# Optimization experiments

Measured on AMD Instinct MI355X. Metric: run time of the kernel, lower is better.

Reference implementation:

```python
import jax, jax.numpy as jnp
import numpy as np

S, B, SD, OD = 10, 256, 16, 8
H = 10 * (SD * SD + OD * OD)        # 3200, gru hidden
OUT1 = 4 * SD * OD                  # 512
IN = 2 * (SD + OD)                  # 48
TEMP = 0.1                          # concrete-dropout temperature


def setup_inputs() -> dict:
    key = jax.random.key(0)
    ks = jax.random.split(key, 24)
    sc = lambda k, sh, s=0.05: jax.random.normal(k, sh, jnp.float32) * s
    return {
        "y_t": sc(ks[0], (B, OD), 1.0),
        "x_filtered_prev": sc(ks[1], (B, SD), 1.0),
        "x_filtered_prev_prev": sc(ks[2], (B, SD), 1.0),
        "y_prev": sc(ks[3], (B, OD), 1.0),
        "delta_x_prev": sc(ks[4], (B, SD), 1.0),
        "h_prev_ensemble": sc(ks[5], (S, B, H)),
        "F_mat": sc(ks[6], (SD, SD), 0.2),
        "H_mat": sc(ks[7], (OD, SD), 0.2),
        "fc_in_w": sc(ks[8], (H, IN)),
        "fc_in_b": jnp.zeros((H,), jnp.float32),
        "W_ih": sc(ks[9], (3 * H, H), 0.01),
        "W_hh": sc(ks[10], (3 * H, H), 0.01),
        "b_ih": jnp.zeros((3 * H,), jnp.float32),
        "b_hh": jnp.zeros((3 * H,), jnp.float32),
        "fc1_w": sc(ks[11], (OUT1, H)),
        "fc1_b": jnp.zeros((OUT1,), jnp.float32),
        "fc2_w": sc(ks[12], (SD * OD, OUT1)),
        "fc2_b": jnp.zeros((SD * OD,), jnp.float32),
        "p_logit1": jnp.array([0.5], jnp.float32),   # sigmoid -> p in (0.5, 0.8) range
        "p_logit2": jnp.array([1.0], jnp.float32),
        "u1": jax.random.uniform(ks[13], (S, B, H), jnp.float32, 1e-4, 1.0 - 1e-4),
        "u2": jax.random.uniform(ks[14], (S, B, OUT1), jnp.float32, 1e-4, 1.0 - 1e-4),
    }


def _concrete_dropout(x, u, p):
    # relaxed Bernoulli drop mask, scaled to keep expectation
    z = jax.nn.sigmoid((jnp.log(p) - jnp.log1p(-p) + jnp.log(u) - jnp.log1p(-u)) / TEMP)
    return x * (1.0 - z) / (1.0 - p)


def reference(y_t, x_filtered_prev, x_filtered_prev_prev, y_prev, delta_x_prev,
              h_prev_ensemble, F_mat, H_mat, fc_in_w, fc_in_b,
              W_ih, W_hh, b_ih, b_hh, fc1_w, fc1_b, fc2_w, fc2_b,
              p_logit1, p_logit2, u1, u2):
    # system model prediction (nonlinear f, linear h), vectorized over batch
    x_predicted = jnp.tanh(x_filtered_prev @ F_mat.T)          # (B, SD)
    y_predicted = x_predicted @ H_mat.T                        # (B, OD)

    residual = y_t - y_predicted
    diff_state = x_filtered_prev - x_filtered_prev_prev
    inp = jnp.concatenate([delta_x_prev, residual, diff_state, y_prev], axis=-1)  # (B, IN)
    a = jax.nn.relu(inp @ fc_in_w.T + fc_in_b)                 # (B, H) shared across ensemble

    p1 = jax.nn.sigmoid(p_logit1[0])
    p2 = jax.nn.sigmoid(p_logit2[0])

    def gru_cell(x, h):
        gx = x @ W_ih.T + b_ih
        gh = h @ W_hh.T + b_hh
        gx_r, gx_z, gx_n = jnp.split(gx, 3, axis=-1)
        gh_r, gh_z, gh_n = jnp.split(gh, 3, axis=-1)
        r = jax.nn.sigmoid(gx_r + gh_r)
        z = jax.nn.sigmoid(gx_z + gh_z)
        n = jnp.tanh(gx_n + r * gh_n)
        return (1.0 - z) * n + z * h

    def sample_fn(h_i, u1_i, u2_i):
        x = _concrete_dropout(a, u1_i, p1)                     # (B, H)
        h_new = gru_cell(x, h_i)                               # (B, H)
        o = jax.nn.relu(h_new @ fc1_w.T + fc1_b)               # (B, OUT1)
        o = _concrete_dropout(o, u2_i, p2)
        K = (o @ fc2_w.T + fc2_b).reshape(B, SD, OD)           # Kalman gain
        correction = jnp.einsum('bso,bo->bs', K, residual)
        return x_predicted + correction, h_new

    xf_ens, h_new_ens = jax.vmap(sample_fn)(h_prev_ensemble, u1, u2)  # (S,B,SD),(S,B,H)

    x_filtered_final = xf_ens.mean(axis=0)                     # (B, SD)
    diff = xf_ens - x_filtered_final                           # (S, B, SD)
    P_filtered_final = jnp.einsum('sbi,sbj->bij', diff, diff) / S

    # concrete-dropout regularizer (identical per ensemble member)
    ent = lambda p: p * jnp.log(p) + (1.0 - p) * jnp.log1p(-p)
    reg = (jnp.sum(fc_in_w ** 2) / (1.0 - p1) + H * ent(p1)
           + jnp.sum(fc1_w ** 2) / (1.0 - p2) + OUT1 * ent(p2))
    raw_regularization = jnp.full((S,), reg)

    return x_filtered_final, P_filtered_final, raw_regularization
```

## Files before the change

### kernel.cpp

```cpp
#include <hip/hip_runtime.h>
#include <hip/hip_bf16.h>
#include <math.h>

#define S_ENS 10
#define B_DIM 256
#define SD 16
#define OD 8
#define H_DIM 3200
#define OUT1 512
#define IN_DIM 48
#define M_ROWS (S_ENS * B_DIM)
#define TEMP_INV 10.0f

typedef unsigned short u16;
typedef __attribute__((ext_vector_type(8))) short short8;
typedef __attribute__((ext_vector_type(4))) short short4v;
typedef __attribute__((ext_vector_type(4))) float floatx4;

__device__ __forceinline__ float sigmoidf_(float x) { return 1.0f / (1.0f + __expf(-x)); }
__device__ __forceinline__ float fast_tanh(float x) {
    x = fminf(fmaxf(x, -15.f), 15.f);
    float e = __expf(2.f * x);
    return (e - 1.f) / (e + 1.f);
}

__device__ __forceinline__ u16 f2bf(float f) {
    union { float f; unsigned u; } v; v.f = f;
    unsigned u = v.u + 0x7fffu + ((v.u >> 16) & 1u);
    return (u16)(u >> 16);
}
__device__ __forceinline__ float bf2f(u16 h) {
    union { unsigned u; float f; } v; v.u = ((unsigned)h) << 16;
    return v.f;
}

__device__ __forceinline__ void gld_lds16(const u16* g, u16* l) {
    __builtin_amdgcn_global_load_lds((const __attribute__((address_space(1))) void*)g,
                                     (__attribute__((address_space(3))) void*)l, 16, 0, 0);
}

__device__ __forceinline__ void bar_() {
    __builtin_amdgcn_sched_barrier(0);
    asm volatile("" ::: "memory");
    __builtin_amdgcn_s_barrier();
    asm volatile("" ::: "memory");
    __builtin_amdgcn_sched_barrier(0);
}
#define VMCNT8() asm volatile("s_waitcnt vmcnt(8)" ::: "memory")

__device__ __forceinline__ void kloop128(
    const u16* __restrict__ A0, const u16* __restrict__ A1,
    const u16* __restrict__ B0, const u16* __restrict__ B1,
    int nts, int nt, int m_base, int n_base,
    u16* sA, u16* sB, floatx4 (&acc)[4][4])
{
    const int tid = threadIdx.x;
    const int wave = tid >> 6, lane = tid & 63;
    const int r = tid >> 2, c = tid & 3;
    const int swe = (c ^ ((r >> 1) & 3)) << 3;
    const int frow = lane & 15, fch = lane >> 4;
    const int wrow0 = (wave >> 1) * 64, wcol0 = (wave & 1) * 64;
    int aoff[4], boff[4];
    #pragma unroll
    for (int mi = 0; mi < 4; ++mi) {
        int row = wrow0 + mi * 16 + frow;
        aoff[mi] = row * 32 + ((fch ^ ((row >> 1) & 3)) << 3);
    }
    #pragma unroll
    for (int ni = 0; ni < 4; ++ni) {
        int row = wcol0 + ni * 16 + frow;
        boff[ni] = row * 32 + ((fch ^ ((row >> 1) & 3)) << 3);
    }

    auto stA = [&](int tau) {
        int tc = tau < nt ? tau : nt - 1;
        const u16* p = (tc < nts) ? A0 : A1;
        int k = ((tc < nts) ? tc : tc - nts) << 6;
        const u16* src = p + (size_t)(m_base + r) * H_DIM + swe + k;
        u16* dst = sA + (tc & 1) * 8192 + wave * 512;
        gld_lds16(src, dst);
        gld_lds16(src + (size_t)64 * H_DIM, dst + 2048);
        gld_lds16(src + 32, dst + 4096);
        gld_lds16(src + 32 + (size_t)64 * H_DIM, dst + 6144);
    };
    auto stB = [&](int tau) {
        int tc = tau < nt ? tau : nt - 1;
        const u16* p = (tc < nts) ? B0 : B1;
        int k = ((tc < nts) ? tc : tc - nts) << 6;
        const u16* src = p + (size_t)(n_base + r) * H_DIM + swe + k;
        u16* dst = sB + (tc & 1) * 8192 + wave * 512;
        gld_lds16(src, dst);
        gld_lds16(src + (size_t)64 * H_DIM, dst + 2048);
        gld_lds16(src + 32, dst + 4096);
        gld_lds16(src + 32 + (size_t)64 * H_DIM, dst + 6144);
    };

    stA(0); stB(0); stA(1); stB(1);
    VMCNT8();
    bar_();

    for (int t = 0; t < nt; ++t) {
        const int bo = (t & 1) * 8192;
        short8 af[4][2], bfr[4][2];
        #pragma unroll
        for (int mi = 0; mi < 4; ++mi) {
            af[mi][0] = *(const short8*)(sA + bo + aoff[mi]);
            af[mi][1] = *(const short8*)(sA + bo + 4096 + aoff[mi]);
        }
        #pragma unroll
        for (int ni = 0; ni < 2; ++ni) {
            bfr[ni][0] = *(const short8*)(sB + bo + boff[ni]);
            bfr[ni][1] = *(const short8*)(sB + bo + 4096 + boff[ni]);
        }
        #pragma unroll
        for (int ni = 2; ni < 4; ++ni) {
            bfr[ni][0] = *(const short8*)(sB + bo + boff[ni]);
            bfr[ni][1] = *(const short8*)(sB + bo + 4096 + boff[ni]);
        }
        bar_();
        __builtin_amdgcn_s_setprio(1);
        #pragma unroll
        for (int mi = 0; mi < 4; ++mi)
            #pragma unroll
            for (int ni = 0; ni < 2; ++ni) {
                acc[mi][ni] = __builtin_amdgcn_mfma_f32_16x16x32_bf16(af[mi][0], bfr[ni][0], acc[mi][ni], 0, 0, 0);
                acc[mi][ni] = __builtin_amdgcn_mfma_f32_16x16x32_bf16(af[mi][1], bfr[ni][1], acc[mi][ni], 0, 0, 0);
            }
        __builtin_amdgcn_s_setprio(0);
        bar_();
        stA(t + 2);
        stB(t + 2);
        __builtin_amdgcn_s_setprio(1);
        #pragma unroll
        for (int mi = 0; mi < 4; ++mi)
            #pragma unroll
            for (int ni = 2; ni < 4; ++ni) {
                acc[mi][ni] = __builtin_amdgcn_mfma_f32_16x16x32_bf16(af[mi][0], bfr[ni][0], acc[mi][ni], 0, 0, 0);
                acc[mi][ni] = __builtin_amdgcn_mfma_f32_16x16x32_bf16(af[mi][1], bfr[ni][1], acc[mi][ni], 0, 0, 0);
            }
        __builtin_amdgcn_s_setprio(0);
        VMCNT8();
        bar_();
    }
}

__global__ __launch_bounds__(256) void gru_gemm_a(
    const u16* __restrict__ Xbf, const u16* __restrict__ Hpbf,
    const u16* __restrict__ Wih, const u16* __restrict__ Whh,
    const float* __restrict__ b_ih, const float* __restrict__ b_hh,
    u16* __restrict__ Rb, u16* __restrict__ Zb, u16* __restrict__ Gb) {
    __shared__ u16 sA[16384], sB[16384];
    floatx4 acc[4][4];
    #pragma unroll
    for (int i = 0; i < 4; ++i)
        #pragma unroll
        for (int j = 0; j < 4; ++j) acc[i][j] = (floatx4){0.f, 0.f, 0.f, 0.f};
    const int g = blockIdx.z;
    const int bmi = blockIdx.x, nbi = blockIdx.y;
    const int m_base = bmi * 128, nb = nbi * 128;
    const size_t gstride = (size_t)H_DIM * H_DIM;
    if (g < 2) {
        kloop128(Xbf, Hpbf, Wih + g * gstride, Whh + g * gstride, 50, 100, m_base, nb, sA, sB, acc);
    } else {
        kloop128(Hpbf, Hpbf, Whh + 2 * gstride, Whh + 2 * gstride, 50, 50, m_base, nb, sA, sB, acc);
    }
    u16* outp = (g == 0) ? Rb : (g == 1) ? Zb : Gb;
    const int lane = threadIdx.x & 63, wave = threadIdx.x >> 6;
    const int wcol0 = (wave & 1) * 64, cc = lane & 15;
    const size_t tbase = (size_t)(nbi * 20 + bmi) * 16384 + wave * 4096 + lane * 4;
    #pragma unroll
    for (int ni = 0; ni < 4; ++ni) {
        int col = nb + wcol0 + ni * 16 + cc;
        float bsum;
        if (g == 0)      bsum = b_ih[col] + b_hh[col];
        else if (g == 1) bsum = b_ih[H_DIM + col] + b_hh[H_DIM + col];
        else             bsum = b_hh[2 * H_DIM + col];
        #pragma unroll
        for (int mi = 0; mi < 4; ++mi) {
            short4v o;
            #pragma unroll
            for (int j = 0; j < 4; ++j) {
                float v = acc[mi][ni][j] + bsum;
                if (g < 2) v = sigmoidf_(v);
                o[j] = (short)f2bf(v);
            }
            *(short4v*)(outp + tbase + (mi * 4 + ni) * 256) = o;
        }
    }
}

__global__ __launch_bounds__(256) void gru_gemm_b(
    const u16* __restrict__ Xbf, const u16* __restrict__ Wih,
    const u16* __restrict__ Rb, const u16* __restrict__ Zb, const u16* __restrict__ Gb,
    const float* __restrict__ b_ih,
    const float* __restrict__ hprev, u16* __restrict__ Hn) {
    __shared__ u16 sA[16384], sB[16384];
    floatx4 acc[4][4];
    #pragma unroll
    for (int i = 0; i < 4; ++i)
        #pragma unroll
        for (int j = 0; j < 4; ++j) acc[i][j] = (floatx4){0.f, 0.f, 0.f, 0.f};
    const int bmi = blockIdx.x, nbi = blockIdx.y;
    const int m_base = bmi * 128, nb = nbi * 128;
    const u16* Wn = Wih + (size_t)2 * H_DIM * H_DIM;
    kloop128(Xbf, Xbf, Wn, Wn, 50, 50, m_base, nb, sA, sB, acc);
    const int lane = threadIdx.x & 63, wave = threadIdx.x >> 6;
    const int wrow0 = (wave >> 1) * 64, wcol0 = (wave & 1) * 64;
    const int quad = lane >> 4, cc = lane & 15;
    const size_t tbase = (size_t)(nbi * 20 + bmi) * 16384 + wave * 4096 + lane * 4;
    #pragma unroll
    for (int ni = 0; ni < 4; ++ni) {
        int col = nb + wcol0 + ni * 16 + cc;
        float bin_ = b_ih[2 * H_DIM + col];
        #pragma unroll
        for (int mi = 0; mi < 4; ++mi) {
            size_t pidx = tbase + (mi * 4 + ni) * 256;
            short4v rv = *(const short4v*)(Rb + pidx);
            short4v zv = *(const short4v*)(Zb + pidx);
            short4v gv = *(const short4v*)(Gb + pidx);
            int rw = m_base + wrow0 + mi * 16 + quad * 4;
            #pragma unroll
            for (int j = 0; j < 4; ++j) {
                float r = bf2f((u16)rv[j]);
                float z = bf2f((u16)zv[j]);
                float gh = bf2f((u16)gv[j]);
                float n = fast_tanh(acc[mi][ni][j] + bin_ + r * gh);
                size_t idx = (size_t)(rw + j) * H_DIM + col;
                float h = hprev[idx];
                Hn[idx] = f2bf((1.f - z) * n + z * h);
            }
        }
    }
}

__global__ __launch_bounds__(256) void fc1_k(
    const u16* __restrict__ Hn, const u16* __restrict__ Wb,
    const float* __restrict__ bias, const float* __restrict__ u2,
    const float* __restrict__ pl2, float* __restrict__ O) {
    __shared__ u16 sA[4096], sB[2048];
    floatx4 acc[4][2];
    #pragma unroll
    for (int i = 0; i < 4; ++i) { acc[i][0] = (floatx4){0.f,0.f,0.f,0.f}; acc[i][1] = (floatx4){0.f,0.f,0.f,0.f}; }
    const int tid = threadIdx.x;
    const int wave = tid >> 6, lane = tid & 63;
    const int m_base = blockIdx.y * 128, nb = blockIdx.x * 64;
    const int r = tid >> 2, c = tid & 3;
    const int swe = (c ^ ((r >> 1) & 3)) << 3;
    const u16* Ag = Hn + (size_t)(m_base + r) * H_DIM + swe;
    const u16* Bg = Wb + (size_t)(nb + r) * H_DIM + swe;
    u16* sA0 = sA + wave * 512;
    u16* sB0 = sB + wave * 512;
    const int frow = lane & 15, fch = lane >> 4;
    const int wrow0 = (wave >> 1) * 64, wcol0 = (wave & 1) * 32;
    int aoff[4], boff[2];
    #pragma unroll
    for (int mi = 0; mi < 4; ++mi) {
        int row = wrow0 + mi * 16 + frow;
        aoff[mi] = row * 32 + ((fch ^ ((row >> 1) & 3)) << 3);
    }
    #pragma unroll
    for (int ni = 0; ni < 2; ++ni) {
        int row = wcol0 + ni * 16 + frow;
        boff[ni] = row * 32 + ((fch ^ ((row >> 1) & 3)) << 3);
    }
    for (int kk = 0; kk < 100; ++kk) {
        __syncthreads();
        gld_lds16(Ag + kk * 32, sA0);
        gld_lds16(Ag + kk * 32 + (size_t)64 * H_DIM, sA0 + 2048);
        gld_lds16(Bg + kk * 32, sB0);
        __syncthreads();
        short8 af[4], bfr[2];
        #pragma unroll
        for (int mi = 0; mi < 4; ++mi) af[mi] = *(const short8*)(sA + aoff[mi]);
        #pragma unroll
        for (int ni = 0; ni < 2; ++ni) bfr[ni] = *(const short8*)(sB + boff[ni]);
        #pragma unroll
        for (int mi = 0; mi < 4; ++mi)
            #pragma unroll
            for (int ni = 0; ni < 2; ++ni)
                acc[mi][ni] = __builtin_amdgcn_mfma_f32_16x16x32_bf16(af[mi], bfr[ni], acc[mi][ni], 0, 0, 0);
    }
    float p = sigmoidf_(pl2[0]);
    float lp = __logf(p) - log1pf(-p);
    float inv = 1.0f / (1.0f - p);
    const int quad = lane >> 4, cc = lane & 15;
    #pragma unroll
    for (int ni = 0; ni < 2; ++ni) {
        int col = nb + wcol0 + ni * 16 + cc;
        float bcol = bias[col];
        #pragma unroll
        for (int mi = 0; mi < 4; ++mi) {
            int rw = m_base + wrow0 + mi * 16 + quad * 4;
            #pragma unroll
            for (int j = 0; j < 4; ++j) {
                size_t idx = (size_t)(rw + j) * OUT1 + col;
                float v = fmaxf(acc[mi][ni][j] + bcol, 0.f);
                float u = u2[idx];
                float z = sigmoidf_((lp + __logf(u) - log1pf(-u)) * TEMP_INV);
                O[idx] = v * (1.0f - z) * inv;
            }
        }
    }
}

__global__ void cvt_bf16_k(const float* __restrict__ src, u16* __restrict__ dst, int n8) {
    int i = blockIdx.x * 256 + threadIdx.x;
    if (i >= n8) return;
    float4 v0 = *((const float4*)src + 2 * (size_t)i);
    float4 v1 = *((const float4*)src + 2 * (size_t)i + 1);
    short8 o;
    o[0] = (short)f2bf(v0.x); o[1] = (short)f2bf(v0.y);
    o[2] = (short)f2bf(v0.z); o[3] = (short)f2bf(v0.w);
    o[4] = (short)f2bf(v1.x); o[5] = (short)f2bf(v1.y);
    o[6] = (short)f2bf(v1.z); o[7] = (short)f2bf(v1.w);
    *(short8*)(dst + 8 * (size_t)i) = o;
}

__global__ void prep_k(const float* __restrict__ y_t, const float* __restrict__ xfp,
                       const float* __restrict__ xfpp, const float* __restrict__ yprev,
                       const float* __restrict__ dxp, const float* __restrict__ Fm,
                       const float* __restrict__ Hm,
                       float* __restrict__ xpred, float* __restrict__ resid,
                       float* __restrict__ inp) {
    int b = threadIdx.x;
    float xrow[SD], xp[SD];
    for (int k = 0; k < SD; ++k) xrow[k] = xfp[b * SD + k];
    for (int s = 0; s < SD; ++s) {
        float acc = 0.f;
        for (int k = 0; k < SD; ++k) acc += xrow[k] * Fm[s * SD + k];
        xp[s] = tanhf(acc);
        xpred[b * SD + s] = xp[s];
    }
    float res[OD];
    for (int o = 0; o < OD; ++o) {
        float acc = 0.f;
        for (int s = 0; s < SD; ++s) acc += xp[s] * Hm[o * SD + s];
        res[o] = y_t[b * OD + o] - acc;
        resid[b * OD + o] = res[o];
    }
    float* ir = inp + b * IN_DIM;
    for (int k = 0; k < SD; ++k) ir[k] = dxp[b * SD + k];
    for (int o = 0; o < OD; ++o) ir[SD + o] = res[o];
    for (int k = 0; k < SD; ++k) ir[SD + OD + k] = xrow[k] - xfpp[b * SD + k];
    for (int o = 0; o < OD; ++o) ir[SD + OD + SD + o] = yprev[b * OD + o];
}

__global__ void fc_in_k(const float* __restrict__ inp, const float* __restrict__ w,
                        const float* __restrict__ bias, float* __restrict__ a) {
    int b = blockIdx.x;
    __shared__ float row[IN_DIM];
    int t = threadIdx.x;
    if (t < IN_DIM) row[t] = inp[b * IN_DIM + t];
    __syncthreads();
    for (int j = t; j < H_DIM; j += 256) {
        float s = bias[j];
        const float* wr = w + j * IN_DIM;
        #pragma unroll 8
        for (int k = 0; k < IN_DIM; ++k) s += row[k] * wr[k];
        a[b * H_DIM + j] = fmaxf(s, 0.f);
    }
}

__global__ void dropx_k(const float* __restrict__ a, const float* __restrict__ u1,
                        const float* __restrict__ pl1, u16* __restrict__ X) {
    int idx_in = blockIdx.x * 256 + threadIdx.x;
    int i = blockIdx.y;
    float p = sigmoidf_(pl1[0]);
    float lp = __logf(p) - log1pf(-p);
    float inv = 1.0f / (1.0f - p);
    size_t gidx = (size_t)i * (B_DIM * H_DIM) + idx_in;
    float u = u1[gidx];
    float z = sigmoidf_((lp + __logf(u) - log1pf(-u)) * TEMP_INV);
    X[gidx] = f2bf(a[idx_in] * (1.0f - z) * inv);
}

__global__ void fc2_corr_k(const float* __restrict__ O, const float* __restrict__ w,
                           const float* __restrict__ bias, const float* __restrict__ resid,
                           const float* __restrict__ xpred, float* __restrict__ xf_ens) {
    int row = blockIdx.x;
    int b = row & (B_DIM - 1);
    __shared__ __align__(16) float orow[OUT1];
    int t = threadIdx.x;
    for (int k = t; k < OUT1; k += 128) orow[k] = O[(size_t)row * OUT1 + k];
    __syncthreads();
    int s = t >> 3, oo = t & 7;
    const float* wr = w + (s * OD + oo) * OUT1;
    float sum = 0.f;
    for (int k = 0; k < OUT1; k += 4) {
        float4 ov = *(const float4*)&orow[k];
        float4 wv = *(const float4*)&wr[k];
        sum += ov.x * wv.x + ov.y * wv.y + ov.z * wv.z + ov.w * wv.w;
    }
    sum += bias[s * OD + oo];
    float v = sum * resid[b * OD + oo];
    v += __shfl_down(v, 4, 8);
    v += __shfl_down(v, 2, 8);
    v += __shfl_down(v, 1, 8);
    if (oo == 0) xf_ens[row * SD + s] = xpred[b * SD + s] + v;
}

__global__ void stats_k(const float* __restrict__ xf_ens, float* __restrict__ out) {
    int b = blockIdx.x;
    __shared__ float xf[S_ENS][SD];
    __shared__ float mean[SD];
    int t = threadIdx.x;
    if (t < S_ENS * SD) {
        int s = t >> 4, k = t & 15;
        xf[s][k] = xf_ens[s * (B_DIM * SD) + b * SD + k];
    }
    __syncthreads();
    if (t < SD) {
        float m = 0.f;
        for (int s = 0; s < S_ENS; ++s) m += xf[s][t];
        m *= (1.0f / S_ENS);
        mean[t] = m;
        out[b * SD + t] = m;
    }
    __syncthreads();
    int i = t >> 4, j = t & 15;
    float p = 0.f;
    for (int s = 0; s < S_ENS; ++s) p += (xf[s][i] - mean[i]) * (xf[s][j] - mean[j]);
    out[B_DIM * SD + b * 256 + t] = p * (1.0f / S_ENS);
}

__global__ void sumsq_k(const float* __restrict__ w, int n, float* __restrict__ accum) {
    float s = 0.f;
    for (int i = blockIdx.x * blockDim.x + threadIdx.x; i < n; i += gridDim.x * blockDim.x) {
        float v = w[i];
        s += v * v;
    }
    #pragma unroll
    for (int d = 32; d >= 1; d >>= 1) s += __shfl_down(s, d, 64);
    __shared__ float red[4];
    int lane = threadIdx.x & 63, wv = threadIdx.x >> 6;
    if (lane == 0) red[wv] = s;
    __syncthreads();
    if (threadIdx.x == 0) atomicAdd(accum, red[0] + red[1] + red[2] + red[3]);
}

__global__ void write_reg_k(const float* __restrict__ sums, const float* __restrict__ pl1,
                            const float* __restrict__ pl2, float* __restrict__ out) {
    int t = threadIdx.x;
    float p1 = sigmoidf_(pl1[0]);
    float p2 = sigmoidf_(pl2[0]);
    float ent1 = p1 * logf(p1) + (1.f - p1) * log1pf(-p1);
    float ent2 = p2 * logf(p2) + (1.f - p2) * log1pf(-p2);
    float reg = sums[0] / (1.f - p1) + (float)H_DIM * ent1
              + sums[1] / (1.f - p2) + (float)OUT1 * ent2;
    if (t < S_ENS) out[B_DIM * SD + B_DIM * SD * SD + t] = reg;
}

extern "C" void kernel_launch(void* const* d_in, const int* in_sizes, int n_in,
                              void* d_out, int out_size, void* d_ws, size_t ws_size,
                              hipStream_t stream) {
    const float* y_t     = (const float*)d_in[0];
    const float* xfp     = (const float*)d_in[1];
    const float* xfpp    = (const float*)d_in[2];
    const float* yprev   = (const float*)d_in[3];
    const float* dxp     = (const float*)d_in[4];
    const float* hprev   = (const float*)d_in[5];
    const float* Fm      = (const float*)d_in[6];
    const float* Hm      = (const float*)d_in[7];
    const float* fc_in_w = (const float*)d_in[8];
    const float* fc_in_b = (const float*)d_in[9];
    const float* W_ih    = (const float*)d_in[10];
    const float* W_hh    = (const float*)d_in[11];
    const float* b_ih    = (const float*)d_in[12];
    const float* b_hh    = (const float*)d_in[13];
    const float* fc1_w   = (const float*)d_in[14];
    const float* fc1_b   = (const float*)d_in[15];
    const float* fc2_w   = (const float*)d_in[16];
    const float* fc2_b   = (const float*)d_in[17];
    const float* pl1     = (const float*)d_in[18];
    const float* pl2     = (const float*)d_in[19];
    const float* u1      = (const float*)d_in[20];
    const float* u2      = (const float*)d_in[21];
    float* out = (float*)d_out;
    char* ws = (char*)d_ws;

    const size_t SZ_W    = (size_t)3 * H_DIM * H_DIM * 2;
    const size_t SZ_MH   = (size_t)M_ROWS * H_DIM * 2;
    size_t off = 0;
    u16* Wihbf  = (u16*)(ws + off); off += SZ_W;
    u16* Whhbf  = (u16*)(ws + off); off += SZ_W;
    u16* Rb     = (u16*)(ws + off); off += SZ_MH;
    u16* Zb     = (u16*)(ws + off); off += SZ_MH;
    u16* Gb     = (u16*)(ws + off); off += SZ_MH;
    u16* Xbf    = (u16*)(ws + off); off += SZ_MH;
    u16* Hpbf   = (u16*)(ws + off); off += SZ_MH;
    u16* Hnbf   = Hpbf;
    u16* fc1wbf = (u16*)(ws + off); off += (size_t)OUT1 * H_DIM * 2;
    float* O_buf   = (float*)(ws + off); off += (size_t)M_ROWS * OUT1 * 4;
    float* a_buf   = (float*)(ws + off); off += (size_t)B_DIM * H_DIM * 4;
    float* xf_buf  = (float*)(ws + off); off += (size_t)M_ROWS * SD * 4;
    float* xpred_b = (float*)(ws + off); off += (size_t)B_DIM * SD * 4;
    float* res_b   = (float*)(ws + off); off += (size_t)B_DIM * OD * 4;
    float* inp_b   = (float*)(ws + off); off += (size_t)B_DIM * IN_DIM * 4;
    float* sums_b  = (float*)(ws + off); off += 256;

    hipMemsetAsync(sums_b, 0, 2 * sizeof(float), stream);

    prep_k<<<1, 256, 0, stream>>>(y_t, xfp, xfpp, yprev, dxp, Fm, Hm, xpred_b, res_b, inp_b);
    fc_in_k<<<B_DIM, 256, 0, stream>>>(inp_b, fc_in_w, fc_in_b, a_buf);
    dropx_k<<<dim3(B_DIM * H_DIM / 256, S_ENS), 256, 0, stream>>>(a_buf, u1, pl1, Xbf);

    cvt_bf16_k<<<15000, 256, 0, stream>>>(W_ih, Wihbf, 3 * H_DIM * H_DIM / 8);
    cvt_bf16_k<<<15000, 256, 0, stream>>>(W_hh, Whhbf, 3 * H_DIM * H_DIM / 8);
    cvt_bf16_k<<<4000, 256, 0, stream>>>(hprev, Hpbf, M_ROWS * H_DIM / 8);
    cvt_bf16_k<<<800, 256, 0, stream>>>(fc1_w, fc1wbf, OUT1 * H_DIM / 8);

    gru_gemm_a<<<dim3(M_ROWS / 128, H_DIM / 128, 3), 256, 0, stream>>>(
        Xbf, Hpbf, Wihbf, Whhbf, b_ih, b_hh, Rb, Zb, Gb);
    gru_gemm_b<<<dim3(M_ROWS / 128, H_DIM / 128), 256, 0, stream>>>(
        Xbf, Wihbf, Rb, Zb, Gb, b_ih, hprev, Hnbf);

    fc1_k<<<dim3(OUT1 / 64, M_ROWS / 128), 256, 0, stream>>>(Hnbf, fc1wbf, fc1_b, u2, pl2, O_buf);

    fc2_corr_k<<<M_ROWS, 128, 0, stream>>>(O_buf, fc2_w, fc2_b, res_b, xpred_b, xf_buf);
    stats_k<<<B_DIM, 256, 0, stream>>>(xf_buf, out);
    sumsq_k<<<256, 256, 0, stream>>>(fc_in_w, H_DIM * IN_DIM, sums_b);
    sumsq_k<<<1024, 256, 0, stream>>>(fc1_w, OUT1 * H_DIM, sums_b + 1);
    write_reg_k<<<1, 64, 0, stream>>>(sums_b, pl1, pl2, out);
}
```

Baseline: 963.5 us.

## Restructure GEMM inner loop and merge small prep, convert and reduction kernels

```diff
diff --git a/kernel.cpp b/kernel.cpp
--- a/kernel.cpp
+++ b/kernel.cpp
@@ -47,6 +47,9 @@
     __builtin_amdgcn_sched_barrier(0);
 }
 #define VMCNT8() asm volatile("s_waitcnt vmcnt(8)" ::: "memory")
+#define LGKM0()  do { __builtin_amdgcn_sched_barrier(0); \
+                      asm volatile("s_waitcnt lgkmcnt(0)" ::: "memory"); \
+                      __builtin_amdgcn_sched_barrier(0); } while (0)
 
 __device__ __forceinline__ void kloop128(
     const u16* __restrict__ A0, const u16* __restrict__ A1,
@@ -108,25 +111,11 @@
             af[mi][1] = *(const short8*)(sA + bo + 4096 + aoff[mi]);
         }
         #pragma unroll
-        for (int ni = 0; ni < 2; ++ni) {
+        for (int ni = 0; ni < 4; ++ni) {
             bfr[ni][0] = *(const short8*)(sB + bo + boff[ni]);
             bfr[ni][1] = *(const short8*)(sB + bo + 4096 + boff[ni]);
         }
-        #pragma unroll
-        for (int ni = 2; ni < 4; ++ni) {
-            bfr[ni][0] = *(const short8*)(sB + bo + boff[ni]);
-            bfr[ni][1] = *(const short8*)(sB + bo + 4096 + boff[ni]);
-        }
-        bar_();
-        __builtin_amdgcn_s_setprio(1);
-        #pragma unroll
-        for (int mi = 0; mi < 4; ++mi)
-            #pragma unroll
-            for (int ni = 0; ni < 2; ++ni) {
-                acc[mi][ni] = __builtin_amdgcn_mfma_f32_16x16x32_bf16(af[mi][0], bfr[ni][0], acc[mi][ni], 0, 0, 0);
-                acc[mi][ni] = __builtin_amdgcn_mfma_f32_16x16x32_bf16(af[mi][1], bfr[ni][1], acc[mi][ni], 0, 0, 0);
-            }
-        __builtin_amdgcn_s_setprio(0);
+        LGKM0();
         bar_();
         stA(t + 2);
         stB(t + 2);
@@ -134,7 +123,7 @@
         #pragma unroll
         for (int mi = 0; mi < 4; ++mi)
             #pragma unroll
-            for (int ni = 2; ni < 4; ++ni) {
+            for (int ni = 0; ni < 4; ++ni) {
                 acc[mi][ni] = __builtin_amdgcn_mfma_f32_16x16x32_bf16(af[mi][0], bfr[ni][0], acc[mi][ni], 0, 0, 0);
                 acc[mi][ni] = __builtin_amdgcn_mfma_f32_16x16x32_bf16(af[mi][1], bfr[ni][1], acc[mi][ni], 0, 0, 0);
             }
@@ -303,54 +292,55 @@
     }
 }
 
-__global__ void cvt_bf16_k(const float* __restrict__ src, u16* __restrict__ dst, int n8) {
-    int i = blockIdx.x * 256 + threadIdx.x;
-    if (i >= n8) return;
-    float4 v0 = *((const float4*)src + 2 * (size_t)i);
-    float4 v1 = *((const float4*)src + 2 * (size_t)i + 1);
+__global__ void cvt4_k(const float* __restrict__ s0, u16* __restrict__ d0,
+                       const float* __restrict__ s1, u16* __restrict__ d1,
+                       const float* __restrict__ s2, u16* __restrict__ d2,
+                       const float* __restrict__ s3, u16* __restrict__ d3) {
+    int blk = blockIdx.x;
+    const float* s; u16* d; size_t i;
+    if (blk < 15000)      { s = s0; d = d0; i = (size_t)blk * 256 + threadIdx.x; }
+    else if (blk < 30000) { s = s1; d = d1; i = (size_t)(blk - 15000) * 256 + threadIdx.x; }
+    else if (blk < 34000) { s = s2; d = d2; i = (size_t)(blk - 30000) * 256 + threadIdx.x; }
+    else                  { s = s3; d = d3; i = (size_t)(blk - 34000) * 256 + threadIdx.x; }
+    float4 v0 = *((const float4*)s + 2 * i);
+    float4 v1 = *((const float4*)s + 2 * i + 1);
     short8 o;
     o[0] = (short)f2bf(v0.x); o[1] = (short)f2bf(v0.y);
     o[2] = (short)f2bf(v0.z); o[3] = (short)f2bf(v0.w);
     o[4] = (short)f2bf(v1.x); o[5] = (short)f2bf(v1.y);
     o[6] = (short)f2bf(v1.z); o[7] = (short)f2bf(v1.w);
-    *(short8*)(dst + 8 * (size_t)i) = o;
-}
-
-__global__ void prep_k(const float* __restrict__ y_t, const float* __restrict__ xfp,
-                       const float* __restrict__ xfpp, const float* __restrict__ yprev,
-                       const float* __restrict__ dxp, const float* __restrict__ Fm,
-                       const float* __restrict__ Hm,
-                       float* __restrict__ xpred, float* __restrict__ resid,
-                       float* __restrict__ inp) {
-    int b = threadIdx.x;
-    float xrow[SD], xp[SD];
-    for (int k = 0; k < SD; ++k) xrow[k] = xfp[b * SD + k];
-    for (int s = 0; s < SD; ++s) {
+    *(short8*)(d + 8 * i) = o;
+}
+
+__global__ void prep_fcin_k(const float* __restrict__ y_t, const float* __restrict__ xfp,
+                            const float* __restrict__ xfpp, const float* __restrict__ yprev,
+                            const float* __restrict__ dxp, const float* __restrict__ Fm,
+                            const float* __restrict__ Hm,
+                            const float* __restrict__ w, const float* __restrict__ bias,
+                            float* __restrict__ xpred, float* __restrict__ resid,
+                            float* __restrict__ a) {
+    int b = blockIdx.x;
+    int t = threadIdx.x;
+    __shared__ float row[IN_DIM];
+    __shared__ float xps[SD];
+    if (t < SD) {
         float acc = 0.f;
-        for (int k = 0; k < SD; ++k) acc += xrow[k] * Fm[s * SD + k];
-        xp[s] = tanhf(acc);
-        xpred[b * SD + s] = xp[s];
-    }
-    float res[OD];
-    for (int o = 0; o < OD; ++o) {
+        for (int k = 0; k < SD; ++k) acc += xfp[b * SD + k] * Fm[t * SD + k];
+        float xp = tanhf(acc);
+        xps[t] = xp;
+        xpred[b * SD + t] = xp;
+        row[t] = dxp[b * SD + t];
+        row[SD + OD + t] = xfp[b * SD + t] - xfpp[b * SD + t];
+    }
+    __syncthreads();
+    if (t < OD) {
         float acc = 0.f;
-        for (int s = 0; s < SD; ++s) acc += xp[s] * Hm[o * SD + s];
-        res[o] = y_t[b * OD + o] - acc;
-        resid[b * OD + o] = res[o];
-    }
-    float* ir = inp + b * IN_DIM;
-    for (int k = 0; k < SD; ++k) ir[k] = dxp[b * SD + k];
-    for (int o = 0; o < OD; ++o) ir[SD + o] = res[o];
-    for (int k = 0; k < SD; ++k) ir[SD + OD + k] = xrow[k] - xfpp[b * SD + k];
-    for (int o = 0; o < OD; ++o) ir[SD + OD + SD + o] = yprev[b * OD + o];
-}
-
-__global__ void fc_in_k(const float* __restrict__ inp, const float* __restrict__ w,
-                        const float* __restrict__ bias, float* __restrict__ a) {
-    int b = blockIdx.x;
-    __shared__ float row[IN_DIM];
-    int t = threadIdx.x;
-    if (t < IN_DIM) row[t] = inp[b * IN_DIM + t];
+        for (int s = 0; s < SD; ++s) acc += xps[s] * Hm[t * SD + s];
+        float res = y_t[b * OD + t] - acc;
+        resid[b * OD + t] = res;
+        row[SD + t] = res;
+        row[SD + OD + SD + t] = yprev[b * OD + t];
+    }
     __syncthreads();
     for (int j = t; j < H_DIM; j += 256) {
         float s = bias[j];
@@ -423,7 +413,11 @@
     out[B_DIM * SD + b * 256 + t] = p * (1.0f / S_ENS);
 }
 
-__global__ void sumsq_k(const float* __restrict__ w, int n, float* __restrict__ accum) {
+__global__ void sumsq2_k(const float* __restrict__ w0, int n0,
+                         const float* __restrict__ w1, int n1,
+                         float* __restrict__ accum) {
+    const float* w = blockIdx.y ? w1 : w0;
+    int n = blockIdx.y ? n1 : n0;
     float s = 0.f;
     for (int i = blockIdx.x * blockDim.x + threadIdx.x; i < n; i += gridDim.x * blockDim.x) {
         float v = w[i];
@@ -435,7 +429,7 @@
     int lane = threadIdx.x & 63, wv = threadIdx.x >> 6;
     if (lane == 0) red[wv] = s;
     __syncthreads();
-    if (threadIdx.x == 0) atomicAdd(accum, red[0] + red[1] + red[2] + red[3]);
+    if (threadIdx.x == 0) atomicAdd(accum + blockIdx.y, red[0] + red[1] + red[2] + red[3]);
 }
 
 __global__ void write_reg_k(const float* __restrict__ sums, const float* __restrict__ pl1,
@@ -495,19 +489,15 @@
     float* xf_buf  = (float*)(ws + off); off += (size_t)M_ROWS * SD * 4;
     float* xpred_b = (float*)(ws + off); off += (size_t)B_DIM * SD * 4;
     float* res_b   = (float*)(ws + off); off += (size_t)B_DIM * OD * 4;
-    float* inp_b   = (float*)(ws + off); off += (size_t)B_DIM * IN_DIM * 4;
     float* sums_b  = (float*)(ws + off); off += 256;
 
     hipMemsetAsync(sums_b, 0, 2 * sizeof(float), stream);
 
-    prep_k<<<1, 256, 0, stream>>>(y_t, xfp, xfpp, yprev, dxp, Fm, Hm, xpred_b, res_b, inp_b);
-    fc_in_k<<<B_DIM, 256, 0, stream>>>(inp_b, fc_in_w, fc_in_b, a_buf);
+    prep_fcin_k<<<B_DIM, 256, 0, stream>>>(y_t, xfp, xfpp, yprev, dxp, Fm, Hm,
+                                           fc_in_w, fc_in_b, xpred_b, res_b, a_buf);
     dropx_k<<<dim3(B_DIM * H_DIM / 256, S_ENS), 256, 0, stream>>>(a_buf, u1, pl1, Xbf);
 
-    cvt_bf16_k<<<15000, 256, 0, stream>>>(W_ih, Wihbf, 3 * H_DIM * H_DIM / 8);
-    cvt_bf16_k<<<15000, 256, 0, stream>>>(W_hh, Whhbf, 3 * H_DIM * H_DIM / 8);
-    cvt_bf16_k<<<4000, 256, 0, stream>>>(hprev, Hpbf, M_ROWS * H_DIM / 8);
-    cvt_bf16_k<<<800, 256, 0, stream>>>(fc1_w, fc1wbf, OUT1 * H_DIM / 8);
+    cvt4_k<<<34800, 256, 0, stream>>>(W_ih, Wihbf, W_hh, Whhbf, hprev, Hpbf, fc1_w, fc1wbf);
 
     gru_gemm_a<<<dim3(M_ROWS / 128, H_DIM / 128, 3), 256, 0, stream>>>(
         Xbf, Hpbf, Wihbf, Whhbf, b_ih, b_hh, Rb, Zb, Gb);
@@ -518,7 +508,6 @@
 
     fc2_corr_k<<<M_ROWS, 128, 0, stream>>>(O_buf, fc2_w, fc2_b, res_b, xpred_b, xf_buf);
     stats_k<<<B_DIM, 256, 0, stream>>>(xf_buf, out);
-    sumsq_k<<<256, 256, 0, stream>>>(fc_in_w, H_DIM * IN_DIM, sums_b);
-    sumsq_k<<<1024, 256, 0, stream>>>(fc1_w, OUT1 * H_DIM, sums_b + 1);
+    sumsq2_k<<<dim3(512, 2), 256, 0, stream>>>(fc_in_w, H_DIM * IN_DIM, fc1_w, OUT1 * H_DIM, sums_b);
     write_reg_k<<<1, 64, 0, stream>>>(sums_b, pl1, pl2, out);
 }
```

Measured after the change: 931.8 us. 1.03x faster.
